# Optimization experiments

Measured on AMD Instinct MI355X. Metric: run time of the kernel, lower is better.

The kernel has to match this reference:

```python
import jax, jax.numpy as jnp
import numpy as np

N = 20000        # nodes
E = 160000       # directed edges (before self loops)
NODE_DIM = 1287
HEADS = 4
C1, C2, C3 = 128, 256, 128
ACT_SLOPE = 0.15   # module's LeakyReLU between layers
GAT_SLOPE = 0.2    # PyG GATConv default negative_slope


def _gat_layer(x, src, dst, W, att_src, att_dst, bias, heads, out_dim, concat):
    # x: [N, in] ; W: [in, heads*out] ; att_*: [heads, out] ; bias: [heads*out] or [out]
    h = (x @ W).reshape(N, heads, out_dim)                      # [N, H, C]
    a_s = jnp.einsum('nhc,hc->nh', h, att_src)                  # [N, H]
    a_d = jnp.einsum('nhc,hc->nh', h, att_dst)                  # [N, H]
    e = jax.nn.leaky_relu(a_s[src] + a_d[dst], GAT_SLOPE)       # [Etot, H]
    # segment softmax over incoming edges of each dst node (self loops => no empty segments)
    m = jax.ops.segment_max(e, dst, num_segments=N)             # [N, H]
    w = jnp.exp(e - m[dst])
    den = jax.ops.segment_sum(w, dst, num_segments=N)           # [N, H]
    alpha = w / den[dst]                                        # [Etot, H]
    msg = h[src] * alpha[:, :, None]                            # [Etot, H, C]
    out = jax.ops.segment_sum(msg, dst, num_segments=N)         # [N, H, C]
    out = out.reshape(N, heads * out_dim) if concat else out.mean(axis=1)
    return out + bias


def setup_inputs() -> dict:
    key = jax.random.key(0)
    ks = jax.random.split(key, 22)
    s = 0.05
    x = jax.random.normal(ks[0], (N, NODE_DIM), jnp.float32)
    edge_index = jax.random.randint(ks[1], (2, E), 0, N, dtype=jnp.int64)
    inp = {
        'x': x, 'edge_index': edge_index,
        'W1': jax.random.normal(ks[2], (NODE_DIM, HEADS * C1), jnp.float32) * s,
        'as1': jax.random.normal(ks[3], (HEADS, C1), jnp.float32) * s,
        'ad1': jax.random.normal(ks[4], (HEADS, C1), jnp.float32) * s,
        'b1': jnp.zeros((HEADS * C1,), jnp.float32),
        'W2': jax.random.normal(ks[5], (HEADS * C1, HEADS * C2), jnp.float32) * s,
        'as2': jax.random.normal(ks[6], (HEADS, C2), jnp.float32) * s,
        'ad2': jax.random.normal(ks[7], (HEADS, C2), jnp.float32) * s,
        'b2': jnp.zeros((HEADS * C2,), jnp.float32),
        # conv3: 1024 -> 128, 1 head, no concat
        'W3': jax.random.normal(ks[8], (HEADS * C2, C3), jnp.float32) * s,
        'as3': jax.random.normal(ks[9], (1, C3), jnp.float32) * s,
        'ad3': jax.random.normal(ks[10], (1, C3), jnp.float32) * s,
        'b3': jnp.zeros((C3,), jnp.float32),
        # pre_fc: 128 -> 16
        'pw': jax.random.normal(ks[11], (C3, 16), jnp.float32) * s,
        'pb': jnp.zeros((16,), jnp.float32),
        # fc fallback: Linear(16,32) -> LeakyReLU(0.15) -> Linear(32,2)
        'f1w': jax.random.normal(ks[12], (16, 32), jnp.float32) * s,
        'f1b': jnp.zeros((32,), jnp.float32),
        'f2w': jax.random.normal(ks[13], (32, 2), jnp.float32) * s,
        'f2b': jnp.zeros((2,), jnp.float32),
    }
    return inp


def reference(x, edge_index, W1, as1, ad1, b1, W2, as2, ad2, b2,
              W3, as3, ad3, b3, pw, pb, f1w, f1b, f2w, f2b):
    loop = jnp.arange(N, dtype=edge_index.dtype)
    src = jnp.concatenate([edge_index[0], loop])   # PyG add_self_loops=True
    dst = jnp.concatenate([edge_index[1], loop])
    h = _gat_layer(x, src, dst, W1, as1, ad1, b1, HEADS, C1, True)
    h = jax.nn.leaky_relu(h, ACT_SLOPE)            # dropout = identity (eval)
    h = _gat_layer(h, src, dst, W2, as2, ad2, b2, HEADS, C2, True)
    h = jax.nn.leaky_relu(h, ACT_SLOPE)
    h = _gat_layer(h, src, dst, W3, as3, ad3, b3, 1, C3, False)
    h = jax.nn.leaky_relu(h, ACT_SLOPE)
    h = h @ pw + pb                                 # pre_fc (128 -> 16)
    h = jax.nn.leaky_relu(h @ f1w + f1b, ACT_SLOPE)
    return h @ f2w + f2b                            # [N, 2] logits
```

## Files before the change

kernel.cpp:

```cpp
#include <hip/hip_runtime.h>
#include <hip/hip_bf16.h>
#include <cstdint>
#include <cstddef>

#define LRELU(x, s) ((x) > 0.f ? (x) : (s) * (x))

typedef __attribute__((ext_vector_type(8))) short bf16x8;
typedef __attribute__((ext_vector_type(4))) float f32x4;

__device__ __forceinline__ float bflo(uint v) { return __uint_as_float(v << 16); }
__device__ __forceinline__ float bfhi(uint v) { return __uint_as_float(v & 0xffff0000u); }
__device__ __forceinline__ ushort f2bf(float f) {
  const uint u = __float_as_uint(f);
  return (ushort)((u + 0x7fffu + ((u >> 16) & 1u)) >> 16);
}

__device__ __forceinline__ void async16(const ushort* g, ushort* l) {
  __builtin_amdgcn_global_load_lds(
      (const __attribute__((address_space(1))) unsigned int*)g,
      (__attribute__((address_space(3))) unsigned int*)l, 16, 0, 0);
}

#define WAITCNT_VM(n) (0xF70 | (n))

__global__ void cast_pad_rows(const float* __restrict__ in, ushort* __restrict__ out,
                              int rows, int K, int Kp) {
  const int P4 = Kp >> 2;
  const long long idx = (long long)blockIdx.x * blockDim.x + threadIdx.x;
  if (idx >= (long long)rows * P4) return;
  const int r = (int)(idx / P4);
  const int c = ((int)(idx - (long long)r * P4)) << 2;
  const float* p = in + (size_t)r * K + c;
  float v0 = 0.f, v1 = 0.f, v2 = 0.f, v3 = 0.f;
  if (c + 3 < K) { v0 = p[0]; v1 = p[1]; v2 = p[2]; v3 = p[3]; }
  else {
    if (c + 0 < K) v0 = p[0];
    if (c + 1 < K) v1 = p[1];
    if (c + 2 < K) v2 = p[2];
    if (c + 3 < K) v3 = p[3];
  }
  uint2 o;
  o.x = (uint)f2bf(v0) | ((uint)f2bf(v1) << 16);
  o.y = (uint)f2bf(v2) | ((uint)f2bf(v3) << 16);
  *(uint2*)(out + (size_t)r * Kp + c) = o;
}

__global__ void cast_W_T(const float* __restrict__ W, ushort* __restrict__ Wt,
                         int K, int Nn, int Kp) {
  __shared__ float tile[32][33];
  const int kt = blockIdx.x * 32;
  const int nt = blockIdx.y * 32;
  const int tx = threadIdx.x;
  const int ty = threadIdx.y;
  for (int r = ty; r < 32; r += 8) {
    const int k = kt + r, nn = nt + tx;
    tile[r][tx] = (k < K && nn < Nn) ? W[(size_t)k * Nn + nn] : 0.f;
  }
  __syncthreads();
  for (int r = ty; r < 32; r += 8) {
    const int nn = nt + r, k = kt + tx;
    if (nn < Nn && k < Kp) Wt[(size_t)nn * Kp + k] = f2bf(tile[tx][r]);
  }
}

template <int TM>
__global__ __launch_bounds__(256) void gemm_bf16(
    const ushort* __restrict__ A, const ushort* __restrict__ Bt, ushort* __restrict__ C,
    int M, int N, int Kp, int Ars,
    const float* __restrict__ AS, const float* __restrict__ AD,
    float* __restrict__ asb, float* __restrict__ adb, int H, int headC) {
  constexpr int MI = TM / 32;
  constexpr int LPG = (TM == 128) ? 4 : 3;
  __shared__ ushort sA[3 * TM * 32];
  __shared__ ushort sB[3 * 128 * 32];
  const int tid = threadIdx.x;
  const int wave = tid >> 6;
  const int lane = tid & 63;
  const int tilesN = N >> 7;
  const int bx = blockIdx.x % tilesN;
  const int by = blockIdx.x / tilesN;
  const int wrow = (wave >> 1) * (TM / 2);
  const int wcol = (wave & 1) * 64;
  const int quad = lane >> 4;
  const int ml = lane & 15;

  const int seg = (lane & 3) * 8;
  const int rB0 = wave * 32 + (lane >> 2);
  const ushort* pB0 = Bt + (size_t)(bx * 128 + rB0) * Kp + seg;
  const ushort* pB1 = Bt + (size_t)(bx * 128 + rB0 + 16) * Kp + seg;
  ushort* lB0 = &sB[(wave * 32) * 32];
  ushort* lB1 = &sB[(wave * 32 + 16) * 32];
  const ushort *pA0, *pA1;
  ushort *lA0, *lA1;
  if constexpr (TM == 128) {
    const int r0 = wave * 32 + (lane >> 2);
    pA0 = A + (size_t)min(by * TM + r0, M - 1) * Ars + seg;
    pA1 = A + (size_t)min(by * TM + r0 + 16, M - 1) * Ars + seg;
    lA0 = &sA[(wave * 32) * 32];
    lA1 = &sA[(wave * 32 + 16) * 32];
  } else {
    const int r0 = wave * 16 + (lane >> 2);
    pA0 = A + (size_t)min(by * TM + r0, M - 1) * Ars + seg;
    pA1 = nullptr;
    lA0 = &sA[(wave * 16) * 32];
    lA1 = nullptr;
  }

  const int nIter = Kp >> 5;
  auto issue = [&](int it, int p) {
    const int k0 = it << 5;
    const int oa = p * TM * 32;
    const int ob_ = p * 128 * 32;
    async16(pA0 + k0, lA0 + oa);
    if constexpr (TM == 128) async16(pA1 + k0, lA1 + oa);
    async16(pB0 + k0, lB0 + ob_);
    async16(pB1 + k0, lB1 + ob_);
  };

  f32x4 acc[MI][4];
#pragma unroll
  for (int mi = 0; mi < MI; mi++)
#pragma unroll
    for (int ni = 0; ni < 4; ni++)
#pragma unroll
      for (int e = 0; e < 4; e++) acc[mi][ni][e] = 0.f;

  issue(0, 0);
  if (nIter > 1) issue(1, 1);
  int p = 0;
  for (int it = 0; it < nIter; ++it) {
    if (it + 1 < nIter) __builtin_amdgcn_s_waitcnt(WAITCNT_VM(LPG));
    else __builtin_amdgcn_s_waitcnt(WAITCNT_VM(0));
    __builtin_amdgcn_s_barrier();
    if (it + 2 < nIter) {
      const int pw = p ? p - 1 : 2;
      issue(it + 2, pw);
    }
    const ushort* bA = &sA[p * TM * 32];
    const ushort* bB = &sB[p * 128 * 32];
    bf16x8 af[MI], bfr[4];
#pragma unroll
    for (int mi = 0; mi < MI; mi++)
      af[mi] = *(const bf16x8*)&bA[(wrow + mi * 16 + ml) * 32 + quad * 8];
#pragma unroll
    for (int ni = 0; ni < 4; ni++)
      bfr[ni] = *(const bf16x8*)&bB[(wcol + ni * 16 + ml) * 32 + quad * 8];
#pragma unroll
    for (int mi = 0; mi < MI; mi++)
#pragma unroll
      for (int ni = 0; ni < 4; ni++)
        acc[mi][ni] = __builtin_amdgcn_mfma_f32_16x16x32_bf16(af[mi], bfr[ni], acc[mi][ni], 0, 0, 0);
    p = (p == 2) ? 0 : p + 1;
  }

#pragma unroll
  for (int mi = 0; mi < MI; mi++) {
#pragma unroll
    for (int r = 0; r < 4; r++) {
      const int row = by * TM + wrow + mi * 16 + quad * 4 + r;
      if (row < M) {
#pragma unroll
        for (int ni = 0; ni < 4; ni++) {
          const int col = bx * 128 + wcol + ni * 16 + ml;
          C[(size_t)row * N + col] = f2bf(acc[mi][ni][r]);
        }
      }
    }
  }

  if (asb != nullptr) {
    float asv[4], adv[4];
#pragma unroll
    for (int ni = 0; ni < 4; ni++) {
      const int col = bx * 128 + wcol + ni * 16 + ml;
      asv[ni] = AS[col];
      adv[ni] = AD[col];
    }
    const int hh = (bx * 128 + wcol) / headC;
#pragma unroll
    for (int mi = 0; mi < MI; mi++) {
#pragma unroll
      for (int r = 0; r < 4; r++) {
        float ps = acc[mi][0][r] * asv[0] + acc[mi][1][r] * asv[1] +
                   acc[mi][2][r] * asv[2] + acc[mi][3][r] * asv[3];
        float pd = acc[mi][0][r] * adv[0] + acc[mi][1][r] * adv[1] +
                   acc[mi][2][r] * adv[2] + acc[mi][3][r] * adv[3];
#pragma unroll
        for (int off = 1; off < 16; off <<= 1) {
          ps += __shfl_xor(ps, off);
          pd += __shfl_xor(pd, off);
        }
        if (ml == 0) {
          const int row = by * TM + wrow + mi * 16 + quad * 4 + r;
          if (row < M) {
            atomicAdd(&asb[row * H + hh], ps);
            atomicAdd(&adb[row * H + hh], pd);
          }
        }
      }
    }
  }
}

__global__ void count_deg(const int* __restrict__ dst, int E, int* __restrict__ deg) {
  const int t = blockIdx.x * blockDim.x + threadIdx.x;
  if (t < E) atomicAdd(&deg[dst[t]], 1);
}

__global__ __launch_bounds__(1024) void scan_kernel(const int* __restrict__ deg,
                                                    int* __restrict__ rowptr,
                                                    int* __restrict__ cursor, int n) {
  __shared__ int swsum[16];
  __shared__ int carry_s;
  const int t = threadIdx.x;
  const int wv = t >> 6, lane = t & 63;
  if (t == 0) carry_s = 0;
  __syncthreads();
  for (int base = 0; base < n; base += 1024) {
    const int i = base + t;
    const int v = (i < n) ? (deg[i] + 1) : 0;
    int sc = v;
#pragma unroll
    for (int off = 1; off < 64; off <<= 1) {
      const int u = __shfl_up(sc, off);
      if (lane >= off) sc += u;
    }
    if (lane == 63) swsum[wv] = sc;
    __syncthreads();
    if (t < 16) {
      int x = swsum[t];
#pragma unroll
      for (int off = 1; off < 16; off <<= 1) {
        const int u = __shfl_up(x, off);
        if (t >= off) x += u;
      }
      swsum[t] = x;
    }
    __syncthreads();
    const int incl = sc + (wv == 0 ? 0 : swsum[wv - 1]) + carry_s;
    if (i < n) { rowptr[i + 1] = incl; cursor[i] = incl - v; }
    if (base == 0 && t == 0) rowptr[0] = 0;
    __syncthreads();
    if (t == 0) carry_s += swsum[15];
    __syncthreads();
  }
}

__global__ void scatter_edges(const int* __restrict__ esrc, const int* __restrict__ edst,
                              int E, int Etot, int* __restrict__ cursor,
                              int* __restrict__ csr_src) {
  const int t = blockIdx.x * blockDim.x + threadIdx.x;
  if (t >= Etot) return;
  int s, d;
  if (t < E) { s = esrc[t]; d = edst[t]; } else { s = t - E; d = s; }
  const int pos = atomicAdd(&cursor[d], 1);
  csr_src[pos] = s;
}

template <int H, int C>
__global__ __launch_bounds__(256) void gat_agg_wave(
    const ushort* __restrict__ hb, const int* __restrict__ rowptr,
    const int* __restrict__ csr_src, const float* __restrict__ a_s,
    const float* __restrict__ a_d, const float* __restrict__ bias,
    ushort* __restrict__ outb, float act_slope, int Nn) {
  constexpr int HC = H * C;
  constexpr int NQ = HC / 8;
  constexpr int PPT = NQ / 64;
  const int n = blockIdx.x * 4 + (threadIdx.x >> 6);
  const int lane = threadIdx.x & 63;
  if (n >= Nn) return;
  float ad_n[H];
#pragma unroll
  for (int h = 0; h < H; h++) ad_n[h] = a_d[n * H + h];
  const int start = rowptr[n], end = rowptr[n + 1];
  float acc[PPT][8];
#pragma unroll
  for (int q = 0; q < PPT; q++)
#pragma unroll
    for (int e = 0; e < 8; e++) acc[q][e] = 0.f;
  float den[H];
#pragma unroll
  for (int h = 0; h < H; h++) den[h] = 0.f;

  for (int base = start; base < end; base += 64) {
    const int cnt = min(64, end - base);
    int s = 0;
    float w[H];
#pragma unroll
    for (int h = 0; h < H; h++) w[h] = 0.f;
    if (lane < cnt) {
      s = csr_src[base + lane];
      float asv[H];
      if constexpr (H == 4) {
        const float4 t4 = *(const float4*)(a_s + s * 4);
        asv[0] = t4.x; asv[1] = t4.y; asv[2] = t4.z; asv[3] = t4.w;
      } else {
        asv[0] = a_s[s];
      }
#pragma unroll
      for (int h = 0; h < H; h++) {
        float lg = asv[h] + ad_n[h];
        lg = LRELU(lg, 0.2f);
        w[h] = __expf(lg);
        den[h] += w[h];
      }
    }
    for (int j = 0; j < cnt; j++) {
      const int sj = __shfl(s, j);
      float wj[H];
#pragma unroll
      for (int h = 0; h < H; h++) wj[h] = __shfl(w[h], j);
      const uint4* hp = (const uint4*)(hb + (size_t)sj * HC);
#pragma unroll
      for (int q = 0; q < PPT; q++) {
        const int iq = q * 64 + lane;
        const uint4 v = hp[iq];
        const float wq = wj[(8 * iq) / C];
        acc[q][0] += wq * bflo(v.x);
        acc[q][1] += wq * bfhi(v.x);
        acc[q][2] += wq * bflo(v.y);
        acc[q][3] += wq * bfhi(v.y);
        acc[q][4] += wq * bflo(v.z);
        acc[q][5] += wq * bfhi(v.z);
        acc[q][6] += wq * bflo(v.w);
        acc[q][7] += wq * bfhi(v.w);
      }
    }
  }
#pragma unroll
  for (int h = 0; h < H; h++) {
#pragma unroll
    for (int off = 1; off < 64; off <<= 1) den[h] += __shfl_xor(den[h], off);
    den[h] = 1.f / den[h];
  }
#pragma unroll
  for (int q = 0; q < PPT; q++) {
    const int iq = q * 64 + lane;
    const int c0 = 8 * iq;
    const float iv = den[c0 / C];
    uint4 o;
    float vv[8];
#pragma unroll
    for (int e = 0; e < 8; e++) vv[e] = LRELU(acc[q][e] * iv + bias[c0 + e], act_slope);
    o.x = (uint)f2bf(vv[0]) | ((uint)f2bf(vv[1]) << 16);
    o.y = (uint)f2bf(vv[2]) | ((uint)f2bf(vv[3]) << 16);
    o.z = (uint)f2bf(vv[4]) | ((uint)f2bf(vv[5]) << 16);
    o.w = (uint)f2bf(vv[6]) | ((uint)f2bf(vv[7]) << 16);
    ((uint4*)outb)[(size_t)n * NQ + iq] = o;
  }
}

__global__ __launch_bounds__(64) void gat_agg3_mlp(
    const ushort* __restrict__ hb, const int* __restrict__ rowptr,
    const int* __restrict__ csr_src, const float* __restrict__ a_s,
    const float* __restrict__ a_d, const float* __restrict__ b3,
    const float* __restrict__ pw, const float* __restrict__ pb,
    const float* __restrict__ f1w, const float* __restrict__ f1b,
    const float* __restrict__ f2w, const float* __restrict__ f2b,
    float* __restrict__ out) {
  const int n = blockIdx.x;
  const int tid = threadIdx.x;
  __shared__ float sx[128];
  __shared__ float s1[16];
  __shared__ float s2[32];
  const float ad_n = a_d[n];
  const int start = rowptr[n], end = rowptr[n + 1];
  float2 acc = make_float2(0.f, 0.f);
  float den = 0.f;
  for (int base = start; base < end; base += 64) {
    const int cnt = min(64, end - base);
    int s = 0;
    float w = 0.f;
    if (tid < cnt) {
      s = csr_src[base + tid];
      float lg = a_s[s] + ad_n;
      lg = LRELU(lg, 0.2f);
      w = __expf(lg);
      den += w;
    }
    for (int j = 0; j < cnt; j++) {
      const int sj = __shfl(s, j);
      const float wj = __shfl(w, j);
      const uint v = ((const uint*)(hb + (size_t)sj * 128))[tid];
      acc.x += wj * bflo(v);
      acc.y += wj * bfhi(v);
    }
  }
#pragma unroll
  for (int off = 1; off < 64; off <<= 1) den += __shfl_xor(den, off);
  const float iv = 1.f / den;
  sx[2 * tid]     = LRELU(acc.x * iv + b3[2 * tid], 0.15f);
  sx[2 * tid + 1] = LRELU(acc.y * iv + b3[2 * tid + 1], 0.15f);
  __syncthreads();
  if (tid < 16) {
    float a = pb[tid];
    for (int c = 0; c < 128; c++) a += sx[c] * pw[c * 16 + tid];
    s1[tid] = a;
  }
  __syncthreads();
  if (tid < 32) {
    float a = f1b[tid];
    for (int c = 0; c < 16; c++) a += s1[c] * f1w[c * 32 + tid];
    s2[tid] = LRELU(a, 0.15f);
  }
  __syncthreads();
  if (tid < 2) {
    float a = f2b[tid];
    for (int c = 0; c < 32; c++) a += s2[c] * f2w[c * 2 + tid];
    out[(size_t)n * 2 + tid] = a;
  }
}

extern "C" void kernel_launch(void* const* d_in, const int* in_sizes, int n_in,
                              void* d_out, int out_size, void* d_ws, size_t ws_size,
                              hipStream_t stream) {
  const float* x   = (const float*)d_in[0];
  const int* ei    = (const int*)d_in[1];
  const float* W1  = (const float*)d_in[2];
  const float* as1 = (const float*)d_in[3];
  const float* ad1 = (const float*)d_in[4];
  const float* b1  = (const float*)d_in[5];
  const float* W2  = (const float*)d_in[6];
  const float* as2 = (const float*)d_in[7];
  const float* ad2 = (const float*)d_in[8];
  const float* b2  = (const float*)d_in[9];
  const float* W3  = (const float*)d_in[10];
  const float* as3 = (const float*)d_in[11];
  const float* ad3 = (const float*)d_in[12];
  const float* b3  = (const float*)d_in[13];
  const float* pw  = (const float*)d_in[14];
  const float* pb  = (const float*)d_in[15];
  const float* f1w = (const float*)d_in[16];
  const float* f1b = (const float*)d_in[17];
  const float* f2w = (const float*)d_in[18];
  const float* f2b = (const float*)d_in[19];
  float* out = (float*)d_out;

  const int N = in_sizes[0] / 1287;
  const int E = in_sizes[1] / 2;
  const int Etot = E + N;
  const int* esrc = ei;
  const int* edst = ei + E;
  const int K1 = 1287, K1p = 1312;

  char* ws = (char*)d_ws;
  size_t off = 0;
  auto alloc = [&](size_t bytes) -> void* {
    void* p = ws + off;
    off = (off + bytes + 255) & ~(size_t)255;
    return p;
  };
  ushort* hb  = (ushort*)alloc((size_t)N * 1024 * 2);
  ushort* ob  = (ushort*)alloc((size_t)N * 1024 * 2);
  ushort* xb  = (ushort*)alloc((size_t)N * K1p * 2);
  ushort* W1t = (ushort*)alloc((size_t)512 * K1p * 2);
  ushort* W2t = (ushort*)alloc((size_t)1024 * 512 * 2);
  ushort* W3t = (ushort*)alloc((size_t)128 * 1024 * 2);
  float* av   = (float*)alloc((size_t)N * 8 * sizeof(float));
  int* deg    = (int*)alloc((size_t)N * sizeof(int));
  int* rowptr = (int*)alloc((size_t)(N + 1) * sizeof(int));
  int* cursor = (int*)alloc((size_t)N * sizeof(int));
  int* csr    = (int*)alloc((size_t)Etot * sizeof(int));
  float* asb = av;
  float* adb = av + (size_t)N * 4;

  hipMemsetAsync(deg, 0, (size_t)N * sizeof(int), stream);
  count_deg<<<(E + 255) / 256, 256, 0, stream>>>(edst, E, deg);
  scan_kernel<<<1, 1024, 0, stream>>>(deg, rowptr, cursor, N);
  scatter_edges<<<(Etot + 255) / 256, 256, 0, stream>>>(esrc, edst, E, Etot, cursor, csr);

  {
    const long long nx = (long long)N * (K1p / 4);
    cast_pad_rows<<<(int)((nx + 255) / 256), 256, 0, stream>>>(x, xb, N, K1, K1p);
    cast_W_T<<<dim3(K1p / 32, (512 + 31) / 32), dim3(32, 8), 0, stream>>>(W1, W1t, K1, 512, K1p);
    cast_W_T<<<dim3(512 / 32, 1024 / 32), dim3(32, 8), 0, stream>>>(W2, W2t, 512, 1024, 512);
    cast_W_T<<<dim3(1024 / 32, 128 / 32), dim3(32, 8), 0, stream>>>(W3, W3t, 1024, 128, 1024);
  }

  const int tilesM = (N + 127) / 128;
  const int tilesM64 = (N + 63) / 64;
  const int nodeBlocks = (N + 3) / 4;

  hipMemsetAsync(av, 0, (size_t)N * 8 * sizeof(float), stream);
  gemm_bf16<128><<<tilesM * 4, 256, 0, stream>>>(xb, W1t, hb, N, 512, K1p, K1p,
                                                 as1, ad1, asb, adb, 4, 128);
  gat_agg_wave<4, 128><<<nodeBlocks, 256, 0, stream>>>(hb, rowptr, csr, asb, adb,
                                                       b1, ob, 0.15f, N);

  hipMemsetAsync(av, 0, (size_t)N * 8 * sizeof(float), stream);
  gemm_bf16<128><<<tilesM * 8, 256, 0, stream>>>(ob, W2t, hb, N, 1024, 512, 512,
                                                 as2, ad2, asb, adb, 4, 256);
  gat_agg_wave<4, 256><<<nodeBlocks, 256, 0, stream>>>(hb, rowptr, csr, asb, adb,
                                                       b2, ob, 0.15f, N);

  hipMemsetAsync(av, 0, (size_t)N * 8 * sizeof(float), stream);
  gemm_bf16<64><<<tilesM64, 256, 0, stream>>>(ob, W3t, hb, N, 128, 1024, 1024,
                                              as3, ad3, asb, adb, 1, 128);
  gat_agg3_mlp<<<N, 64, 0, stream>>>(hb, rowptr, csr, asb, adb, b3,
                                     pw, pb, f1w, f1b, f2w, f2b, out);
}
```

Baseline: 527.6 us.

## Use 128x256 tiles with 512-thread blocks for layer 1 and 2 GEMMs

Replaces the templated 128x128 GEMM for the first two layers with a 512-thread kernel computing 128x256 output tiles. It uses a unified double-buffered LDS stage where each wave loads three 16-row slices of A or B. A wider N tile halves the A re-reads from global memory and gives more MFMA work per barrier. The cost is fewer blocks, an extra barrier per iteration because there are only two buffers, and a larger LDS footprint. The layer-3 GEMM keeps the old 64-row path as a separate non-templated kernel.

New measurement: 530.6 us. About the same (+0.6%).

```diff
diff --git a/kernel.cpp b/kernel.cpp
--- a/kernel.cpp
+++ b/kernel.cpp
@@ -63,15 +63,140 @@
   }
 }
 
-template <int TM>
-__global__ __launch_bounds__(256) void gemm_bf16(
+__global__ __launch_bounds__(512) void gemm_wide(
     const ushort* __restrict__ A, const ushort* __restrict__ Bt, ushort* __restrict__ C,
     int M, int N, int Kp, int Ars,
     const float* __restrict__ AS, const float* __restrict__ AD,
     float* __restrict__ asb, float* __restrict__ adb, int H, int headC) {
-  constexpr int MI = TM / 32;
-  constexpr int LPG = (TM == 128) ? 4 : 3;
-  __shared__ ushort sA[3 * TM * 32];
+  constexpr int ROWS = 384;
+  __shared__ ushort sAB[2 * ROWS * 32];
+  const int tid = threadIdx.x;
+  const int wave = tid >> 6;
+  const int lane = tid & 63;
+  const int tilesN = N >> 8;
+  const int bx = blockIdx.x % tilesN;
+  const int by = blockIdx.x / tilesN;
+  const int wrow = (wave >> 2) * 64;
+  const int wcol = (wave & 3) * 64;
+  const int quad = lane >> 4;
+  const int ml = lane & 15;
+
+  const int seg = (lane & 3) * 8;
+  const ushort* gp[3];
+  int lo[3];
+  const int rsub = lane >> 2;
+#pragma unroll
+  for (int i = 0; i < 3; i++) {
+    const int base = wave * 48 + i * 16;
+    lo[i] = base * 32;
+    if (base < 128) {
+      const int g = base + rsub;
+      gp[i] = A + (size_t)min(by * 128 + g, M - 1) * Ars + seg;
+    } else {
+      const int b = base - 128 + rsub;
+      gp[i] = Bt + (size_t)(bx * 256 + b) * Kp + seg;
+    }
+  }
+
+  const int nIter = Kp >> 5;
+  auto issue = [&](int it, int p) {
+    const int k0 = it << 5;
+    const int po = p * (ROWS * 32);
+#pragma unroll
+    for (int i = 0; i < 3; i++) async16(gp[i] + k0, &sAB[po + lo[i]]);
+  };
+
+  f32x4 acc[4][4];
+#pragma unroll
+  for (int mi = 0; mi < 4; mi++)
+#pragma unroll
+    for (int ni = 0; ni < 4; ni++)
+#pragma unroll
+      for (int e = 0; e < 4; e++) acc[mi][ni][e] = 0.f;
+
+  issue(0, 0);
+  if (nIter > 1) issue(1, 1);
+  int p = 0;
+  for (int it = 0; it < nIter; ++it) {
+    if (it + 1 < nIter) __builtin_amdgcn_s_waitcnt(WAITCNT_VM(3));
+    else __builtin_amdgcn_s_waitcnt(WAITCNT_VM(0));
+    __builtin_amdgcn_s_barrier();
+    const ushort* bA = &sAB[p * (ROWS * 32)];
+    const ushort* bB = bA + 128 * 32;
+    bf16x8 af[4], bfr[4];
+#pragma unroll
+    for (int mi = 0; mi < 4; mi++)
+      af[mi] = *(const bf16x8*)&bA[(wrow + mi * 16 + ml) * 32 + quad * 8];
+#pragma unroll
+    for (int ni = 0; ni < 4; ni++)
+      bfr[ni] = *(const bf16x8*)&bB[(wcol + ni * 16 + ml) * 32 + quad * 8];
+#pragma unroll
+    for (int mi = 0; mi < 4; mi++)
+#pragma unroll
+      for (int ni = 0; ni < 4; ni++)
+        acc[mi][ni] = __builtin_amdgcn_mfma_f32_16x16x32_bf16(af[mi], bfr[ni], acc[mi][ni], 0, 0, 0);
+    if (it + 2 < nIter) {
+      __builtin_amdgcn_s_barrier();
+      issue(it + 2, p);
+    }
+    p ^= 1;
+  }
+
+#pragma unroll
+  for (int mi = 0; mi < 4; mi++) {
+#pragma unroll
+    for (int r = 0; r < 4; r++) {
+      const int row = by * 128 + wrow + mi * 16 + quad * 4 + r;
+      if (row < M) {
+#pragma unroll
+        for (int ni = 0; ni < 4; ni++) {
+          const int col = bx * 256 + wcol + ni * 16 + ml;
+          C[(size_t)row * N + col] = f2bf(acc[mi][ni][r]);
+        }
+      }
+    }
+  }
+
+  if (asb != nullptr) {
+    float asv[4], adv[4];
+#pragma unroll
+    for (int ni = 0; ni < 4; ni++) {
+      const int col = bx * 256 + wcol + ni * 16 + ml;
+      asv[ni] = AS[col];
+      adv[ni] = AD[col];
+    }
+    const int hh = (bx * 256 + wcol) / headC;
+#pragma unroll
+    for (int mi = 0; mi < 4; mi++) {
+#pragma unroll
+      for (int r = 0; r < 4; r++) {
+        float ps = acc[mi][0][r] * asv[0] + acc[mi][1][r] * asv[1] +
+                   acc[mi][2][r] * asv[2] + acc[mi][3][r] * asv[3];
+        float pd = acc[mi][0][r] * adv[0] + acc[mi][1][r] * adv[1] +
+                   acc[mi][2][r] * adv[2] + acc[mi][3][r] * adv[3];
+#pragma unroll
+        for (int off = 1; off < 16; off <<= 1) {
+          ps += __shfl_xor(ps, off);
+          pd += __shfl_xor(pd, off);
+        }
+        if (ml == 0) {
+          const int row = by * 128 + wrow + mi * 16 + quad * 4 + r;
+          if (row < M) {
+            atomicAdd(&asb[row * H + hh], ps);
+            atomicAdd(&adb[row * H + hh], pd);
+          }
+        }
+      }
+    }
+  }
+}
+
+__global__ __launch_bounds__(256) void gemm64(
+    const ushort* __restrict__ A, const ushort* __restrict__ Bt, ushort* __restrict__ C,
+    int M, int N, int Kp, int Ars,
+    const float* __restrict__ AS, const float* __restrict__ AD,
+    float* __restrict__ asb, float* __restrict__ adb, int H, int headC) {
+  __shared__ ushort sA[3 * 64 * 32];
   __shared__ ushort sB[3 * 128 * 32];
   const int tid = threadIdx.x;
   const int wave = tid >> 6;
@@ -79,7 +204,7 @@
   const int tilesN = N >> 7;
   const int bx = blockIdx.x % tilesN;
   const int by = blockIdx.x / tilesN;
-  const int wrow = (wave >> 1) * (TM / 2);
+  const int wrow = (wave >> 1) * 32;
   const int wcol = (wave & 1) * 64;
   const int quad = lane >> 4;
   const int ml = lane & 15;
@@ -90,36 +215,21 @@
   const ushort* pB1 = Bt + (size_t)(bx * 128 + rB0 + 16) * Kp + seg;
   ushort* lB0 = &sB[(wave * 32) * 32];
   ushort* lB1 = &sB[(wave * 32 + 16) * 32];
-  const ushort *pA0, *pA1;
-  ushort *lA0, *lA1;
-  if constexpr (TM == 128) {
-    const int r0 = wave * 32 + (lane >> 2);
-    pA0 = A + (size_t)min(by * TM + r0, M - 1) * Ars + seg;
-    pA1 = A + (size_t)min(by * TM + r0 + 16, M - 1) * Ars + seg;
-    lA0 = &sA[(wave * 32) * 32];
-    lA1 = &sA[(wave * 32 + 16) * 32];
-  } else {
-    const int r0 = wave * 16 + (lane >> 2);
-    pA0 = A + (size_t)min(by * TM + r0, M - 1) * Ars + seg;
-    pA1 = nullptr;
-    lA0 = &sA[(wave * 16) * 32];
-    lA1 = nullptr;
-  }
+  const int r0 = wave * 16 + (lane >> 2);
+  const ushort* pA0 = A + (size_t)min(by * 64 + r0, M - 1) * Ars + seg;
+  ushort* lA0 = &sA[(wave * 16) * 32];
 
   const int nIter = Kp >> 5;
   auto issue = [&](int it, int p) {
     const int k0 = it << 5;
-    const int oa = p * TM * 32;
-    const int ob_ = p * 128 * 32;
-    async16(pA0 + k0, lA0 + oa);
-    if constexpr (TM == 128) async16(pA1 + k0, lA1 + oa);
-    async16(pB0 + k0, lB0 + ob_);
-    async16(pB1 + k0, lB1 + ob_);
+    async16(pA0 + k0, lA0 + p * 64 * 32);
+    async16(pB0 + k0, lB0 + p * 128 * 32);
+    async16(pB1 + k0, lB1 + p * 128 * 32);
   };
 
-  f32x4 acc[MI][4];
-#pragma unroll
-  for (int mi = 0; mi < MI; mi++)
+  f32x4 acc[2][4];
+#pragma unroll
+  for (int mi = 0; mi < 2; mi++)
 #pragma unroll
     for (int ni = 0; ni < 4; ni++)
 #pragma unroll
@@ -129,24 +239,24 @@
   if (nIter > 1) issue(1, 1);
   int p = 0;
   for (int it = 0; it < nIter; ++it) {
-    if (it + 1 < nIter) __builtin_amdgcn_s_waitcnt(WAITCNT_VM(LPG));
+    if (it + 1 < nIter) __builtin_amdgcn_s_waitcnt(WAITCNT_VM(3));
     else __builtin_amdgcn_s_waitcnt(WAITCNT_VM(0));
     __builtin_amdgcn_s_barrier();
     if (it + 2 < nIter) {
       const int pw = p ? p - 1 : 2;
       issue(it + 2, pw);
     }
-    const ushort* bA = &sA[p * TM * 32];
+    const ushort* bA = &sA[p * 64 * 32];
     const ushort* bB = &sB[p * 128 * 32];
-    bf16x8 af[MI], bfr[4];
-#pragma unroll
-    for (int mi = 0; mi < MI; mi++)
+    bf16x8 af[2], bfr[4];
+#pragma unroll
+    for (int mi = 0; mi < 2; mi++)
       af[mi] = *(const bf16x8*)&bA[(wrow + mi * 16 + ml) * 32 + quad * 8];
 #pragma unroll
     for (int ni = 0; ni < 4; ni++)
       bfr[ni] = *(const bf16x8*)&bB[(wcol + ni * 16 + ml) * 32 + quad * 8];
 #pragma unroll
-    for (int mi = 0; mi < MI; mi++)
+    for (int mi = 0; mi < 2; mi++)
 #pragma unroll
       for (int ni = 0; ni < 4; ni++)
         acc[mi][ni] = __builtin_amdgcn_mfma_f32_16x16x32_bf16(af[mi], bfr[ni], acc[mi][ni], 0, 0, 0);
@@ -154,10 +264,10 @@
   }
 
 #pragma unroll
-  for (int mi = 0; mi < MI; mi++) {
+  for (int mi = 0; mi < 2; mi++) {
 #pragma unroll
     for (int r = 0; r < 4; r++) {
-      const int row = by * TM + wrow + mi * 16 + quad * 4 + r;
+      const int row = by * 64 + wrow + mi * 16 + quad * 4 + r;
       if (row < M) {
 #pragma unroll
         for (int ni = 0; ni < 4; ni++) {
@@ -178,7 +288,7 @@
     }
     const int hh = (bx * 128 + wcol) / headC;
 #pragma unroll
-    for (int mi = 0; mi < MI; mi++) {
+    for (int mi = 0; mi < 2; mi++) {
 #pragma unroll
       for (int r = 0; r < 4; r++) {
         float ps = acc[mi][0][r] * asv[0] + acc[mi][1][r] * asv[1] +
@@ -191,7 +301,7 @@
           pd += __shfl_xor(pd, off);
         }
         if (ml == 0) {
-          const int row = by * TM + wrow + mi * 16 + quad * 4 + r;
+          const int row = by * 64 + wrow + mi * 16 + quad * 4 + r;
           if (row < M) {
             atomicAdd(&asb[row * H + hh], ps);
             atomicAdd(&adb[row * H + hh], pd);
@@ -482,20 +592,20 @@
   const int nodeBlocks = (N + 3) / 4;
 
   hipMemsetAsync(av, 0, (size_t)N * 8 * sizeof(float), stream);
-  gemm_bf16<128><<<tilesM * 4, 256, 0, stream>>>(xb, W1t, hb, N, 512, K1p, K1p,
-                                                 as1, ad1, asb, adb, 4, 128);
+  gemm_wide<<<tilesM * 2, 512, 0, stream>>>(xb, W1t, hb, N, 512, K1p, K1p,
+                                            as1, ad1, asb, adb, 4, 128);
   gat_agg_wave<4, 128><<<nodeBlocks, 256, 0, stream>>>(hb, rowptr, csr, asb, adb,
                                                        b1, ob, 0.15f, N);
 
   hipMemsetAsync(av, 0, (size_t)N * 8 * sizeof(float), stream);
-  gemm_bf16<128><<<tilesM * 8, 256, 0, stream>>>(ob, W2t, hb, N, 1024, 512, 512,
-                                                 as2, ad2, asb, adb, 4, 256);
+  gemm_wide<<<tilesM * 4, 512, 0, stream>>>(ob, W2t, hb, N, 1024, 512, 512,
+                                            as2, ad2, asb, adb, 4, 256);
   gat_agg_wave<4, 256><<<nodeBlocks, 256, 0, stream>>>(hb, rowptr, csr, asb, adb,
                                                        b2, ob, 0.15f, N);
 
   hipMemsetAsync(av, 0, (size_t)N * 8 * sizeof(float), stream);
-  gemm_bf16<64><<<tilesM64, 256, 0, stream>>>(ob, W3t, hb, N, 128, 1024, 1024,
-                                              as3, ad3, asb, adb, 1, 128);
+  gemm64<<<tilesM64, 256, 0, stream>>>(ob, W3t, hb, N, 128, 1024, 1024,
+                                       as3, ad3, asb, adb, 1, 128);
   gat_agg3_mlp<<<N, 64, 0, stream>>>(hb, rowptr, csr, asb, adb, b3,
                                      pw, pb, f1w, f1b, f2w, f2b, out);
 }
```
